# Optimization experiments

Measured on AMD Instinct MI355X. Metric: run time of the kernel, lower is better.

## Reference

```python
import jax, jax.numpy as jnp
import numpy as np

D_MODEL = 1024
D_INNER = 2048
D_STATE = 16
D_CONV = 4
DT_RANK = 128  # ceil(d_inner/16)
B, L = 4, 2048


def setup_inputs() -> dict:
    key = jax.random.key(0)
    ks = jax.random.split(key, 12)
    s = 0.02
    return {
        "x": jax.random.normal(ks[0], (B, L, D_MODEL), jnp.float32),
        "in_proj_w": jax.random.normal(ks[1], (2 * D_INNER, D_MODEL), jnp.float32) * s,
        "in_proj_b": jax.random.normal(ks[2], (2 * D_INNER,), jnp.float32) * s,
        "conv_w": jax.random.normal(ks[3], (D_INNER, 1, D_CONV), jnp.float32) * s,
        "conv_b": jax.random.normal(ks[4], (D_INNER,), jnp.float32) * s,
        "x_proj_w": jax.random.normal(ks[5], (DT_RANK + 2 * D_STATE, D_INNER), jnp.float32) * s,
        "dt_proj_w": jax.random.normal(ks[6], (D_INNER, DT_RANK), jnp.float32) * s,
        "dt_proj_b": jax.random.normal(ks[7], (D_INNER,), jnp.float32) * s,
        "A_log": jnp.log(jnp.tile(jnp.arange(1, D_STATE + 1, dtype=jnp.float32)[None, :], (D_INNER, 1))),
        "D": jnp.ones((D_INNER,), jnp.float32),
        "out_proj_w": jax.random.normal(ks[8], (D_MODEL, D_INNER), jnp.float32) * s,
        "out_proj_b": jax.random.normal(ks[9], (D_MODEL,), jnp.float32) * s,
    }


def _selective_scan(u, delta, A, B_ssm, C, Dp):
    # u, delta: [b, l, d]; B_ssm, C: [b, l, n]; A: [d, n]; Dp: [d]
    def step(h, inp):
        dlt, Bt, Ct, ut = inp  # [b,d],[b,n],[b,n],[b,d]
        dA = jnp.exp(dlt[..., None] * A)               # [b,d,n]
        dBu = dlt[..., None] * Bt[:, None, :] * ut[..., None]
        h = dA * h + dBu
        y = jnp.einsum('bdn,bn->bd', h, Ct)
        return h, y

    h0 = jnp.zeros((u.shape[0], A.shape[0], A.shape[1]), u.dtype)
    xs = (jnp.swapaxes(delta, 0, 1), jnp.swapaxes(B_ssm, 0, 1),
          jnp.swapaxes(C, 0, 1), jnp.swapaxes(u, 0, 1))
    _, ys = jax.lax.scan(step, h0, xs)                 # [l,b,d]
    return jnp.swapaxes(ys, 0, 1) + u * Dp             # [b,l,d]


def reference(x, in_proj_w, in_proj_b, conv_w, conv_b, x_proj_w,
              dt_proj_w, dt_proj_b, A_log, D, out_proj_w, out_proj_b):
    xr = x @ in_proj_w.T + in_proj_b                   # [b,l,2d]
    xc, res = jnp.split(xr, 2, axis=-1)
    # depthwise conv1d, torch padding='same' with k=4 -> pad (1, 2)
    xcl = jnp.swapaxes(xc, 1, 2)                       # [b,d,l]
    xcl = jax.lax.conv_general_dilated(
        xcl, conv_w, window_strides=(1,), padding=[(1, 2)],
        feature_group_count=D_INNER,
        dimension_numbers=('NCH', 'OIH', 'NCH')) + conv_b[None, :, None]
    xc = jnp.swapaxes(xcl, 1, 2)                       # [b,l,d]
    x_dbl = xc @ x_proj_w.T                            # [b,l,dt_rank+2n]
    d_dt, B_ssm, C = jnp.split(x_dbl, [DT_RANK, DT_RANK + D_STATE], axis=-1)
    delta = jax.nn.softplus(d_dt @ dt_proj_w.T + dt_proj_b)
    A = -jnp.exp(A_log)
    y = _selective_scan(xc, delta, A, B_ssm, C, D)     # [b,l,d]
    y = y * jax.nn.silu(res)
    return y @ out_proj_w.T + out_proj_b
```

## Files before the change

### kernel.cpp

```cpp
#include <hip/hip_runtime.h>
#include <hip/hip_bf16.h>
#include <hip/hip_fp16.h>


typedef _Float16 f16;
typedef __attribute__((ext_vector_type(4))) float f32x4;
typedef __attribute__((ext_vector_type(4))) _Float16 f16x4;
typedef __attribute__((ext_vector_type(8))) _Float16 f16x8;

#define AS1C(p) ((const __attribute__((address_space(1))) void*)(p))
#define AS3(p)  ((__attribute__((address_space(3))) void*)(p))

#define D_MODEL 1024
#define D_INNER 2048
#define LSEQ    2048
#define NB      4
#define NCH     32
#define CLEN    64
#define LOG2E   1.44269504f

__global__ void cvt_f32_to_f16(const float* __restrict__ in, f16* __restrict__ out, int n4) {
  int i = blockIdx.x * blockDim.x + threadIdx.x;
  if (i >= n4) return;
  f32x4 v = *(const f32x4*)(in + (size_t)i * 4);
  f16x4 o;
  o[0] = (f16)v[0]; o[1] = (f16)v[1]; o[2] = (f16)v[2]; o[3] = (f16)v[3];
  *(f16x4*)(out + (size_t)i * 4) = o;
}

__global__ void cvt_pad_xproj(const float* __restrict__ in, f16* __restrict__ out) {
  int i = blockIdx.x * blockDim.x + threadIdx.x;
  int idx = i << 2;
  int row = idx >> 11;
  f16x4 o;
  if (row < 160) {
    f32x4 v = *(const f32x4*)(in + idx);
    o[0] = (f16)v[0]; o[1] = (f16)v[1]; o[2] = (f16)v[2]; o[3] = (f16)v[3];
  } else {
    o[0] = (f16)0.f; o[1] = (f16)0.f; o[2] = (f16)0.f; o[3] = (f16)0.f;
  }
  *(f16x4*)(out + idx) = o;
}

template<int EPI>
__global__ __launch_bounds__(256) void gemm_f16(
    const f16* __restrict__ A, int lda,
    const f16* __restrict__ Bw, int K,
    const float* __restrict__ bias,
    void* __restrict__ O0, void* __restrict__ O1,
    int NV, int ldo)
{
  __shared__ f16 lA[128 * 32];
  __shared__ f16 lB[128 * 32];
  const int tid  = threadIdx.x;
  const int lane = tid & 63;
  const int wid  = tid >> 6;
  const int wr = wid >> 1, wc = wid & 1;
  const int tm = blockIdx.y * 128, tn = blockIdx.x * 128;

  f32x4 acc[4][4] = {};

  const int i4 = lane >> 2;
  const int k8 = (lane & 3) << 3;
  const int ca = wid << 1;
  const f16* Abase = A  + (size_t)(tm + ca * 16 + i4) * lda + k8;
  const f16* Bbase = Bw + (size_t)(tn + ca * 16 + i4) * K   + k8;

  const int nKT = K >> 5;
  for (int kt = 0; kt < nKT; ++kt) {
    const int ko = kt << 5;
    __syncthreads();
    __builtin_amdgcn_global_load_lds(AS1C(Abase + ko),                    AS3(lA + ca * 512),       16, 0, 0);
    __builtin_amdgcn_global_load_lds(AS1C(Abase + (size_t)16 * lda + ko), AS3(lA + ca * 512 + 512), 16, 0, 0);
    __builtin_amdgcn_global_load_lds(AS1C(Bbase + ko),                    AS3(lB + ca * 512),       16, 0, 0);
    __builtin_amdgcn_global_load_lds(AS1C(Bbase + (size_t)16 * K + ko),   AS3(lB + ca * 512 + 512), 16, 0, 0);
    __syncthreads();

    const int ro = lane & 15;
    const int kf = (lane >> 4) << 3;
    f16x8 af[4], bf[4];
#pragma unroll
    for (int mi = 0; mi < 4; ++mi)
      af[mi] = *(const f16x8*)(lA + (wr * 64 + mi * 16 + ro) * 32 + kf);
#pragma unroll
    for (int nj = 0; nj < 4; ++nj)
      bf[nj] = *(const f16x8*)(lB + (wc * 64 + nj * 16 + ro) * 32 + kf);
#pragma unroll
    for (int mi = 0; mi < 4; ++mi)
#pragma unroll
      for (int nj = 0; nj < 4; ++nj)
        acc[mi][nj] = __builtin_amdgcn_mfma_f32_16x16x32_f16(af[mi], bf[nj], acc[mi][nj], 0, 0, 0);
  }

#pragma unroll
  for (int mi = 0; mi < 4; ++mi) {
    const int rb = tm + wr * 64 + mi * 16 + ((lane >> 4) << 2);
#pragma unroll
    for (int nj = 0; nj < 4; ++nj) {
      const int gn = tn + wc * 64 + nj * 16 + (lane & 15);
      if (gn >= NV) continue;
      float bv = 0.f;
      if constexpr (EPI != 1) bv = bias[gn];
#pragma unroll
      for (int j = 0; j < 4; ++j) {
        const float v = acc[mi][nj][j] + bv;
        const size_t row = (size_t)(rb + j);
        if constexpr (EPI == 0) {
          if (gn < 2048) ((f16*)O0)[row * 2048 + gn] = (f16)v;
          else           ((f16*)O1)[row * 2048 + (gn - 2048)] = (f16)v;
        } else if constexpr (EPI == 1) {
          ((f16*)O0)[row * (size_t)ldo + gn] = (f16)v;
        } else if constexpr (EPI == 2) {
          const float sp = (v > 20.f) ? v : log1pf(__expf(v));
          ((f16*)O0)[row * (size_t)ldo + gn] = (f16)sp;
        } else {
          ((float*)O0)[row * (size_t)ldo + gn] = v;
        }
      }
    }
  }
}

__global__ __launch_bounds__(256) void conv1d_kernel(
    const f16* __restrict__ xin, const float* __restrict__ w,
    const float* __restrict__ cb, f16* __restrict__ xout)
{
  const int d0  = threadIdx.x << 3;
  const int bid = blockIdx.x;
  const int b   = bid >> 8;
  const int l0  = (bid & 255) << 3;
  float wv[4][8];
#pragma unroll
  for (int q = 0; q < 8; ++q) {
    f32x4 t = *(const f32x4*)(w + (size_t)(d0 + q) * 4);
    wv[0][q] = t[0]; wv[1][q] = t[1]; wv[2][q] = t[2]; wv[3][q] = t[3];
  }
  float bv[8];
  *(f32x4*)bv       = *(const f32x4*)(cb + d0);
  *(f32x4*)(bv + 4) = *(const f32x4*)(cb + d0 + 4);
  const size_t base = (size_t)b * LSEQ * D_INNER;
  for (int lt = l0; lt < l0 + 8; ++lt) {
    float acc[8];
#pragma unroll
    for (int q = 0; q < 8; ++q) acc[q] = bv[q];
#pragma unroll
    for (int j = 0; j < 4; ++j) {
      const int li = lt + j - 1;
      if (li < 0 || li >= LSEQ) continue;
      f16x8 v = *(const f16x8*)(xin + base + (size_t)li * D_INNER + d0);
#pragma unroll
      for (int q = 0; q < 8; ++q) acc[q] += wv[j][q] * (float)v[q];
    }
    f16x8 o;
#pragma unroll
    for (int q = 0; q < 8; ++q) o[q] = (f16)acc[q];
    *(f16x8*)(xout + base + (size_t)lt * D_INNER + d0) = o;
  }
}


__global__ __launch_bounds__(256) void scan_pass1(
    const f16* __restrict__ delta, const f16* __restrict__ u,
    const f16* __restrict__ xdbl, const float* __restrict__ A_log,
    float* __restrict__ chunkS, float* __restrict__ chunkH)
{
  const int tid = threadIdx.x;
  const int d = blockIdx.x * 256 + tid;
  const int c = blockIdx.y;
  const int b = blockIdx.z;
  __shared__ float bl[CLEN][16];
  {
    const int t = tid >> 2, q = tid & 3;
    if (q < 2) {
      f16x8 v = *(const f16x8*)(xdbl + ((size_t)(b * LSEQ + c * CLEN + t)) * 160 + 128 + q * 8);
      float* dst = &bl[t][q * 8];
#pragma unroll
      for (int e = 0; e < 8; ++e) dst[e] = (float)v[e];
    }
  }
  __syncthreads();

  float An2[16], h[16];
  const float* alp = A_log + (size_t)d * 16;
#pragma unroll
  for (int n = 0; n < 16; ++n) { An2[n] = -__expf(alp[n]) * LOG2E; h[n] = 0.f; }

  float dsum = 0.f;
  size_t off = ((size_t)(b * LSEQ + c * CLEN)) * D_INNER + d;
  float dlt = (float)delta[off];
  float uu  = (float)u[off];
  for (int t = 0; t < CLEN; ++t) {
    float ndlt = 0.f, nuu = 0.f;
    const size_t noff = off + D_INNER;
    if (t < CLEN - 1) { ndlt = (float)delta[noff]; nuu = (float)u[noff]; }
    const float du = dlt * uu;
    dsum += dlt;
#pragma unroll
    for (int n = 0; n < 16; ++n) {
      const float dA = __builtin_amdgcn_exp2f(An2[n] * dlt);
      h[n] = dA * h[n] + du * bl[t][n];
    }
    dlt = ndlt; uu = nuu; off = noff;
  }
  const size_t sb = ((size_t)b * NCH + c) * D_INNER + d;
  chunkS[sb] = dsum;
  const size_t ob = sb * 16;
#pragma unroll
  for (int q = 0; q < 4; ++q) {
    f32x4 vh;
#pragma unroll
    for (int j = 0; j < 4; ++j) vh[j] = h[q * 4 + j];
    *(f32x4*)(chunkH + ob + q * 4) = vh;
  }
}

__global__ __launch_bounds__(256) void scan_combine(
    const float* __restrict__ chunkS, const float* __restrict__ A_log,
    float* __restrict__ chunkH)
{
  const int i = blockIdx.x * 256 + threadIdx.x;
  const int b = i >> 15;
  const int dn = i & 32767;
  const int d = dn >> 4;
  const float An2 = -__expf(A_log[dn]) * LOG2E;
  const size_t hstride = (size_t)D_INNER * 16;
  size_t sIdx = (size_t)b * NCH * D_INNER + d;
  size_t hIdx = ((size_t)b * NCH * D_INNER) * 16 + dn;
  float hin = 0.f;
  for (int c = 0; c < NCH; ++c) {
    const float P  = __builtin_amdgcn_exp2f(An2 * chunkS[sIdx]);
    const float he = chunkH[hIdx];
    chunkH[hIdx] = hin;
    hin = P * hin + he;
    sIdx += D_INNER; hIdx += hstride;
  }
}

__global__ __launch_bounds__(256) void scan_pass2(
    const f16* __restrict__ delta, const f16* __restrict__ u,
    const f16* __restrict__ xdbl, const f16* __restrict__ res,
    const float* __restrict__ A_log, const float* __restrict__ Dp,
    const float* __restrict__ chunkH, f16* __restrict__ yg)
{
  const int tid = threadIdx.x;
  const int d = blockIdx.x * 256 + tid;
  const int c = blockIdx.y;
  const int b = blockIdx.z;
  __shared__ float bl[CLEN][16];
  __shared__ float cl[CLEN][16];
  {
    const int t = tid >> 2, q = tid & 3;
    f16x8 v = *(const f16x8*)(xdbl + ((size_t)(b * LSEQ + c * CLEN + t)) * 160 + 128 + q * 8);
    float* dst = (q < 2) ? &bl[t][(q & 1) * 8] : &cl[t][(q & 1) * 8];
#pragma unroll
    for (int e = 0; e < 8; ++e) dst[e] = (float)v[e];
  }
  __syncthreads();

  float An2[16], h[16];
  const float* alp = A_log + (size_t)d * 16;
#pragma unroll
  for (int n = 0; n < 16; ++n) An2[n] = -__expf(alp[n]) * LOG2E;
  const size_t hb = (((size_t)b * NCH + c) * D_INNER + d) * 16;
#pragma unroll
  for (int q = 0; q < 4; ++q) {
    f32x4 v = *(const f32x4*)(chunkH + hb + q * 4);
#pragma unroll
    for (int j = 0; j < 4; ++j) h[q * 4 + j] = v[j];
  }
  const float Dd = Dp[d];

  size_t off = ((size_t)(b * LSEQ + c * CLEN)) * D_INNER + d;
  float dlt = (float)delta[off];
  float uu  = (float)u[off];
  float rr  = (float)res[off];
  for (int t = 0; t < CLEN; ++t) {
    float ndlt = 0.f, nuu = 0.f, nrr = 0.f;
    const size_t noff = off + D_INNER;
    if (t < CLEN - 1) {
      ndlt = (float)delta[noff]; nuu = (float)u[noff]; nrr = (float)res[noff];
    }
    const float du = dlt * uu;
    float y0 = 0.f, y1 = 0.f, y2 = 0.f, y3 = 0.f;
#pragma unroll
    for (int q = 0; q < 4; ++q) {
      float yp = 0.f;
#pragma unroll
      for (int e = 0; e < 4; ++e) {
        const int n = q * 4 + e;
        const float dA = __builtin_amdgcn_exp2f(An2[n] * dlt);
        h[n] = dA * h[n] + du * bl[t][n];
        yp += h[n] * cl[t][n];
      }
      if (q == 0) y0 = yp; else if (q == 1) y1 = yp; else if (q == 2) y2 = yp; else y3 = yp;
    }
    const float y = (y0 + y1) + (y2 + y3) + uu * Dd;
    const float sil = rr / (1.f + __expf(-rr));
    yg[off] = (f16)(y * sil);
    dlt = ndlt; uu = nuu; rr = nrr; off = noff;
  }
}

extern "C" void kernel_launch(void* const* d_in, const int* in_sizes, int n_in,
                              void* d_out, int out_size, void* d_ws, size_t ws_size,
                              hipStream_t stream) {
  const float* x      = (const float*)d_in[0];
  const float* w_in_f = (const float*)d_in[1];
  const float* b_in   = (const float*)d_in[2];
  const float* conv_w = (const float*)d_in[3];
  const float* conv_b = (const float*)d_in[4];
  const float* w_xp_f = (const float*)d_in[5];
  const float* w_dt_f = (const float*)d_in[6];
  const float* b_dt   = (const float*)d_in[7];
  const float* A_log  = (const float*)d_in[8];
  const float* Dp     = (const float*)d_in[9];
  const float* w_ot_f = (const float*)d_in[10];
  const float* b_ot   = (const float*)d_in[11];

  char* ws = (char*)d_ws;
  size_t o = 0;
  auto alloc = [&](size_t bytes) -> char* {
    char* p = ws + o; o += (bytes + 255) & ~(size_t)255; return p;
  };
  f16* xf    = (f16*)alloc(16777216);
  f16* w_in  = (f16*)alloc(8388608);
  f16* w_xp  = (f16*)alloc(1048576);
  f16* w_dt  = (f16*)alloc(524288);
  f16* w_ot  = (f16*)alloc(4194304);
  f16* xcr   = (f16*)alloc(33554432);
  f16* res   = (f16*)alloc(33554432);
  f16* xc    = (f16*)alloc(33554432);
  f16* xdbl  = (f16*)alloc(2621440);
  f16* delta = (f16*)alloc(33554432);

  float* chunkH = (float*)xf;
  float* chunkS = (float*)w_in;

  dim3 blk(256);
  cvt_f32_to_f16<<<8192, blk, 0, stream>>>(x,      xf,   2097152);
  cvt_f32_to_f16<<<4096, blk, 0, stream>>>(w_in_f, w_in, 1048576);
  cvt_pad_xproj <<<512,  blk, 0, stream>>>(w_xp_f, w_xp);
  cvt_f32_to_f16<<<256,  blk, 0, stream>>>(w_dt_f, w_dt, 65536);
  cvt_f32_to_f16<<<2048, blk, 0, stream>>>(w_ot_f, w_ot, 524288);

  gemm_f16<0><<<dim3(32, 64), blk, 0, stream>>>(xf, 1024, w_in, 1024, b_in,
                                                xcr, res, 4096, 2048);
  conv1d_kernel<<<1024, blk, 0, stream>>>(xcr, conv_w, conv_b, xc);
  gemm_f16<1><<<dim3(2, 64), blk, 0, stream>>>(xc, 2048, w_xp, 2048, nullptr,
                                               xdbl, nullptr, 160, 160);
  gemm_f16<2><<<dim3(16, 64), blk, 0, stream>>>(xdbl, 160, w_dt, 128, b_dt,
                                                delta, nullptr, 2048, 2048);
  scan_pass1  <<<dim3(8, NCH, NB), blk, 0, stream>>>(delta, xc, xdbl, A_log,
                                                     chunkS, chunkH);
  scan_combine<<<512, blk, 0, stream>>>(chunkS, A_log, chunkH);
  scan_pass2  <<<dim3(8, NCH, NB), blk, 0, stream>>>(delta, xc, xdbl, res,
                                                     A_log, Dp, chunkH, xcr);
  gemm_f16<3><<<dim3(8, 64), blk, 0, stream>>>(xcr, 2048, w_ot, 2048, b_ot,
                                               d_out, nullptr, 1024, 1024);
}
```

Baseline: 429.5 us.

## Remap GEMM blocks per XCD and batch scan loads four steps ahead

The GEMM launches switch from 2D grids to a 1D grid. For the in-projection and out-projection GEMMs, block IDs are remapped so that the blocks landing on each of the 8 XCDs work on a contiguous band of N-tiles, which should improve L2 reuse of weight tiles. Both scan passes now prefetch delta, u and res four timesteps at a time instead of one, to expose more memory-level parallelism in the sequential loop. This raises register pressure, and the swizzle assumes blocks are dispatched round-robin across XCDs and that gx divides by 8.

```diff
diff --git a/kernel.cpp b/kernel.cpp
--- a/kernel.cpp
+++ b/kernel.cpp
@@ -42,13 +42,13 @@
   *(f16x4*)(out + idx) = o;
 }
 
-template<int EPI>
+template<int EPI, bool XSW>
 __global__ __launch_bounds__(256) void gemm_f16(
     const f16* __restrict__ A, int lda,
     const f16* __restrict__ Bw, int K,
     const float* __restrict__ bias,
     void* __restrict__ O0, void* __restrict__ O1,
-    int NV, int ldo)
+    int NV, int ldo, int gx)
 {
   __shared__ f16 lA[128 * 32];
   __shared__ f16 lB[128 * 32];
@@ -56,7 +56,22 @@
   const int lane = tid & 63;
   const int wid  = tid >> 6;
   const int wr = wid >> 1, wc = wid & 1;
-  const int tm = blockIdx.y * 128, tn = blockIdx.x * 128;
+
+  int tn_i, tm_i;
+  {
+    const int bid = blockIdx.x;
+    if constexpr (XSW) {
+      const int nxs = gx >> 3;
+      const int xcd = bid & 7;
+      const int j   = bid >> 3;
+      tn_i = xcd * nxs + j % nxs;
+      tm_i = j / nxs;
+    } else {
+      tn_i = bid % gx;
+      tm_i = bid / gx;
+    }
+  }
+  const int tm = tm_i * 128, tn = tn_i * 128;
 
   f32x4 acc[4][4] = {};
 
@@ -186,21 +201,36 @@
   for (int n = 0; n < 16; ++n) { An2[n] = -__expf(alp[n]) * LOG2E; h[n] = 0.f; }
 
   float dsum = 0.f;
-  size_t off = ((size_t)(b * LSEQ + c * CLEN)) * D_INNER + d;
-  float dlt = (float)delta[off];
-  float uu  = (float)u[off];
-  for (int t = 0; t < CLEN; ++t) {
-    float ndlt = 0.f, nuu = 0.f;
-    const size_t noff = off + D_INNER;
-    if (t < CLEN - 1) { ndlt = (float)delta[noff]; nuu = (float)u[noff]; }
-    const float du = dlt * uu;
-    dsum += dlt;
-#pragma unroll
-    for (int n = 0; n < 16; ++n) {
-      const float dA = __builtin_amdgcn_exp2f(An2[n] * dlt);
-      h[n] = dA * h[n] + du * bl[t][n];
-    }
-    dlt = ndlt; uu = nuu; off = noff;
+  const size_t base = ((size_t)(b * LSEQ + c * CLEN)) * D_INNER + d;
+  float dl[4], uu[4];
+#pragma unroll
+  for (int j = 0; j < 4; ++j) {
+    dl[j] = (float)delta[base + (size_t)j * D_INNER];
+    uu[j] = (float)u[base + (size_t)j * D_INNER];
+  }
+  for (int g = 0; g < CLEN / 4; ++g) {
+    float ndl[4] = {0.f, 0.f, 0.f, 0.f}, nuu[4] = {0.f, 0.f, 0.f, 0.f};
+    if (g < CLEN / 4 - 1) {
+      const size_t nb = base + (size_t)(g + 1) * 4 * D_INNER;
+#pragma unroll
+      for (int j = 0; j < 4; ++j) {
+        ndl[j] = (float)delta[nb + (size_t)j * D_INNER];
+        nuu[j] = (float)u[nb + (size_t)j * D_INNER];
+      }
+    }
+#pragma unroll
+    for (int j = 0; j < 4; ++j) {
+      const int t = g * 4 + j;
+      const float du = dl[j] * uu[j];
+      dsum += dl[j];
+#pragma unroll
+      for (int n = 0; n < 16; ++n) {
+        const float dA = __builtin_amdgcn_exp2f(An2[n] * dl[j]);
+        h[n] = dA * h[n] + du * bl[t][n];
+      }
+    }
+#pragma unroll
+    for (int j = 0; j < 4; ++j) { dl[j] = ndl[j]; uu[j] = nuu[j]; }
   }
   const size_t sb = ((size_t)b * NCH + c) * D_INNER + d;
   chunkS[sb] = dsum;
@@ -270,34 +300,49 @@
   }
   const float Dd = Dp[d];
 
-  size_t off = ((size_t)(b * LSEQ + c * CLEN)) * D_INNER + d;
-  float dlt = (float)delta[off];
-  float uu  = (float)u[off];
-  float rr  = (float)res[off];
-  for (int t = 0; t < CLEN; ++t) {
-    float ndlt = 0.f, nuu = 0.f, nrr = 0.f;
-    const size_t noff = off + D_INNER;
-    if (t < CLEN - 1) {
-      ndlt = (float)delta[noff]; nuu = (float)u[noff]; nrr = (float)res[noff];
-    }
-    const float du = dlt * uu;
-    float y0 = 0.f, y1 = 0.f, y2 = 0.f, y3 = 0.f;
-#pragma unroll
-    for (int q = 0; q < 4; ++q) {
-      float yp = 0.f;
-#pragma unroll
-      for (int e = 0; e < 4; ++e) {
-        const int n = q * 4 + e;
-        const float dA = __builtin_amdgcn_exp2f(An2[n] * dlt);
-        h[n] = dA * h[n] + du * bl[t][n];
-        yp += h[n] * cl[t][n];
+  const size_t base = ((size_t)(b * LSEQ + c * CLEN)) * D_INNER + d;
+  float dl[4], uu[4], rr[4];
+#pragma unroll
+  for (int j = 0; j < 4; ++j) {
+    dl[j] = (float)delta[base + (size_t)j * D_INNER];
+    uu[j] = (float)u[base + (size_t)j * D_INNER];
+    rr[j] = (float)res[base + (size_t)j * D_INNER];
+  }
+  for (int g = 0; g < CLEN / 4; ++g) {
+    float ndl[4] = {0.f, 0.f, 0.f, 0.f}, nuu[4] = {0.f, 0.f, 0.f, 0.f},
+          nrr[4] = {0.f, 0.f, 0.f, 0.f};
+    if (g < CLEN / 4 - 1) {
+      const size_t nb = base + (size_t)(g + 1) * 4 * D_INNER;
+#pragma unroll
+      for (int j = 0; j < 4; ++j) {
+        ndl[j] = (float)delta[nb + (size_t)j * D_INNER];
+        nuu[j] = (float)u[nb + (size_t)j * D_INNER];
+        nrr[j] = (float)res[nb + (size_t)j * D_INNER];
       }
-      if (q == 0) y0 = yp; else if (q == 1) y1 = yp; else if (q == 2) y2 = yp; else y3 = yp;
-    }
-    const float y = (y0 + y1) + (y2 + y3) + uu * Dd;
-    const float sil = rr / (1.f + __expf(-rr));
-    yg[off] = (f16)(y * sil);
-    dlt = ndlt; uu = nuu; rr = nrr; off = noff;
+    }
+#pragma unroll
+    for (int j = 0; j < 4; ++j) {
+      const int t = g * 4 + j;
+      const float du = dl[j] * uu[j];
+      float y0 = 0.f, y1 = 0.f, y2 = 0.f, y3 = 0.f;
+#pragma unroll
+      for (int q = 0; q < 4; ++q) {
+        float yp = 0.f;
+#pragma unroll
+        for (int e = 0; e < 4; ++e) {
+          const int n = q * 4 + e;
+          const float dA = __builtin_amdgcn_exp2f(An2[n] * dl[j]);
+          h[n] = dA * h[n] + du * bl[t][n];
+          yp += h[n] * cl[t][n];
+        }
+        if (q == 0) y0 = yp; else if (q == 1) y1 = yp; else if (q == 2) y2 = yp; else y3 = yp;
+      }
+      const float y = (y0 + y1) + (y2 + y3) + uu[j] * Dd;
+      const float sil = rr[j] / (1.f + __expf(-rr[j]));
+      yg[base + (size_t)t * D_INNER] = (f16)(y * sil);
+    }
+#pragma unroll
+    for (int j = 0; j < 4; ++j) { dl[j] = ndl[j]; uu[j] = nuu[j]; rr[j] = nrr[j]; }
   }
 }
 
@@ -343,18 +388,18 @@
   cvt_f32_to_f16<<<256,  blk, 0, stream>>>(w_dt_f, w_dt, 65536);
   cvt_f32_to_f16<<<2048, blk, 0, stream>>>(w_ot_f, w_ot, 524288);
 
-  gemm_f16<0><<<dim3(32, 64), blk, 0, stream>>>(xf, 1024, w_in, 1024, b_in,
-                                                xcr, res, 4096, 2048);
+  gemm_f16<0, true><<<2048, blk, 0, stream>>>(xf, 1024, w_in, 1024, b_in,
+                                              xcr, res, 4096, 2048, 32);
   conv1d_kernel<<<1024, blk, 0, stream>>>(xcr, conv_w, conv_b, xc);
-  gemm_f16<1><<<dim3(2, 64), blk, 0, stream>>>(xc, 2048, w_xp, 2048, nullptr,
-                                               xdbl, nullptr, 160, 160);
-  gemm_f16<2><<<dim3(16, 64), blk, 0, stream>>>(xdbl, 160, w_dt, 128, b_dt,
-                                                delta, nullptr, 2048, 2048);
+  gemm_f16<1, false><<<128, blk, 0, stream>>>(xc, 2048, w_xp, 2048, nullptr,
+                                              xdbl, nullptr, 160, 160, 2);
+  gemm_f16<2, false><<<1024, blk, 0, stream>>>(xdbl, 160, w_dt, 128, b_dt,
+                                               delta, nullptr, 2048, 2048, 16);
   scan_pass1  <<<dim3(8, NCH, NB), blk, 0, stream>>>(delta, xc, xdbl, A_log,
                                                      chunkS, chunkH);
   scan_combine<<<512, blk, 0, stream>>>(chunkS, A_log, chunkH);
   scan_pass2  <<<dim3(8, NCH, NB), blk, 0, stream>>>(delta, xc, xdbl, res,
                                                      A_log, Dp, chunkH, xcr);
-  gemm_f16<3><<<dim3(8, 64), blk, 0, stream>>>(xcr, 2048, w_ot, 2048, b_ot,
-                                               d_out, nullptr, 1024, 1024);
-}
+  gemm_f16<3, true><<<512, blk, 0, stream>>>(xcr, 2048, w_ot, 2048, b_ot,
+                                             d_out, nullptr, 1024, 1024, 8);
+}
```

New measurement: 419.6 us. 2.3% less time.
